# Optimization experiments

Measured on AMD Instinct MI355X. Metric: run time of the kernel, lower is better.

Reference implementation:

```python
import jax, jax.numpy as jnp
import numpy as np
from itertools import permutations

BLOCK = 64  # GroupLinear block_size


def _dist_bucket_table():
    # replicates self.distance: log2-style bucketing of token distances [0,1024)
    t = np.zeros(1024, dtype=np.int32)
    for i, th in enumerate([2, 4, 8, 16, 32, 64, 128, 256, 512]):
        t[th:] = i + 1
    return jnp.asarray(t)


def setup_inputs() -> dict:
    key = jax.random.key(0)
    ks = jax.random.split(key, 12)
    B, S, H, NH = 4, 512, 768, 12
    E, TAG, TE, TD, R = 24, 7, 20, 20, 97
    DIN = 2 * H + TE + TD
    hidden_state = jax.random.normal(ks[0], (B, S, H), jnp.float32)
    attention = jax.random.uniform(ks[1], (B, NH, S, S), jnp.float32)
    attention_mask = jnp.ones((B, S), jnp.float32)
    head = jnp.sort(jax.random.randint(ks[2], (B, E), 0, S), axis=-1)
    tail = jnp.sort(jax.random.randint(ks[3], (B, E), 0, S), axis=-1)
    entity_type = jax.random.randint(ks[4], (B, E), 0, TAG)
    type_table = jax.random.normal(ks[5], (TAG, TE), jnp.float32) * 0.02
    dis_table = jax.random.normal(ks[6], (20, TD), jnp.float32) * 0.02
    Wh = jax.random.normal(ks[7], (DIN, H), jnp.float32) * (1.0 / np.sqrt(DIN))
    bh = jnp.zeros((H,), jnp.float32)
    Wt = jax.random.normal(ks[8], (DIN, H), jnp.float32) * (1.0 / np.sqrt(DIN))
    bt = jnp.zeros((H,), jnp.float32)
    # GroupLinear weight reshaped to [n_blocks, BLOCK, BLOCK, R]
    clsW = jax.random.normal(ks[9], (H // BLOCK, BLOCK, BLOCK, R), jnp.float32) * (1.0 / np.sqrt(H * BLOCK))
    clsb = jnp.zeros((R,), jnp.float32)
    return dict(hidden_state=hidden_state, attention=attention,
                attention_mask=attention_mask, head=head, tail=tail,
                entity_type=entity_type, type_table=type_table,
                dis_table=dis_table, Wh=Wh, bh=bh, Wt=Wt, bt=bt,
                clsW=clsW, clsb=clsb)


def reference(hidden_state, attention, attention_mask, head, tail, entity_type,
              type_table, dis_table, Wh, bh, Wt, bt, clsW, clsb):
    E = head.shape[1]
    hts = jnp.asarray(list(permutations(range(E), 2)), dtype=jnp.int32)  # [P,2]
    i0, i1 = hts[:, 0], hts[:, 1]
    dtab = _dist_bucket_table()
    att = attention.sum(axis=1)  # [B,S,S] sum over heads

    def per_sample(h, a, m, hd, tl, et):
        # h:[S,H] a:[S,S] m:[S] hd,tl,et:[E]
        ent_feat = (h[hd] + h[tl]) * 0.5          # [E,H]
        ent_att = (a[hd] + a[tl]) * 0.5           # [E,S]
        ent_tf = type_table[et]                   # [E,TE]
        head_f, tail_f = ent_feat[i0], ent_feat[i1]      # [P,H]
        ht_att = ent_att[i0] * ent_att[i1] * m[None, :]  # [P,S]
        head_ty, tail_ty = ent_tf[i0], ent_tf[i1]        # [P,TE]
        d = dtab[jnp.abs(tl[i0] - hd[i1])]               # [P]
        ht_dist = dis_table[d]                           # [P,TD]
        ht_att = ht_att / (ht_att.sum(-1, keepdims=True) + 1e-20)
        ht_info = ht_att @ h                             # [P,H]
        all_h = jnp.concatenate([head_f, ht_info, head_ty, ht_dist], axis=-1)
        all_t = jnp.concatenate([tail_f, ht_info, tail_ty, ht_dist], axis=-1)
        return all_h, all_t

    all_h, all_t = jax.vmap(per_sample)(hidden_state, att, attention_mask,
                                        head, tail, entity_type)
    all_h = all_h.reshape(-1, all_h.shape[-1])  # [B*P, DIN]
    all_t = all_t.reshape(-1, all_t.shape[-1])
    h1 = jnp.tanh(all_h @ Wh + bh)              # [L,H]
    t1 = jnp.tanh(all_t @ Wt + bt)
    L, H = h1.shape
    nb = H // BLOCK
    x1 = h1.reshape(L, nb, BLOCK)
    x2 = t1.reshape(L, nb, BLOCK)
    # GroupLinear: per-block outer product then linear, fused as einsum
    logits = jnp.einsum('lnb,lnc,nbcr->lr', x1, x2, clsW) + clsb  # [L,R]
    return logits
```

## Files before the change

### kernel.cpp

```cpp
#include <hip/hip_runtime.h>
#include <hip/hip_bf16.h>
#include <math.h>

#define B_ 4
#define S_ 512
#define H_ 768
#define NH_ 12
#define E_ 24
#define TE_ 20
#define TD_ 20
#define R_ 97
#define DIN_ 1576
#define KPAD_ 1600
#define KS_MLP 50
#define KS_HTI 16
#define P_ 552
#define L_ 2208
#define NB_ 12
#define NF_ 7

typedef __bf16 bf16x8 __attribute__((ext_vector_type(8)));
typedef float f32x4 __attribute__((ext_vector_type(4)));

__device__ __forceinline__ unsigned short f2bf(float f) {
  union { float f; unsigned u; } c; c.f = f;
  unsigned r = c.u + 0x7FFF + ((c.u >> 16) & 1);
  return (unsigned short)(r >> 16);
}
__device__ __forceinline__ float bf2f(unsigned short b) {
  union { unsigned u; float f; } c; c.u = ((unsigned)b) << 16;
  return c.f;
}
__device__ __forceinline__ unsigned pk2(float a, float b) {
  return (unsigned)f2bf(a) | ((unsigned)f2bf(b) << 16);
}
__device__ __forceinline__ void gload_lds16(const uint4* g, uint4* l) {
  __builtin_amdgcn_global_load_lds(
      (const __attribute__((address_space(1))) unsigned*)(const void*)g,
      (__attribute__((address_space(3))) unsigned*)(void*)l, 16, 0, 0);
}

__global__ void ent_prep(const float* __restrict__ attn, const float* __restrict__ hs,
                         const int* __restrict__ head, const int* __restrict__ tail,
                         float* __restrict__ ent_att, float* __restrict__ ent_feat) {
  int be = blockIdx.x;
  int b = be / E_;
  int hd = head[be], tl = tail[be];
  int tid = threadIdx.x;
  const float* abase = attn + (size_t)b * NH_ * S_ * S_;
  for (int s = tid; s < S_; s += 256) {
    float acc = 0.f;
#pragma unroll
    for (int nh = 0; nh < NH_; ++nh) {
      const float* ap = abase + (size_t)nh * S_ * S_;
      acc += ap[(size_t)hd * S_ + s] + ap[(size_t)tl * S_ + s];
    }
    ent_att[(size_t)be * S_ + s] = 0.5f * acc;
  }
  const float* hb = hs + (size_t)b * S_ * H_;
  for (int k = tid; k < H_; k += 256) {
    ent_feat[(size_t)be * H_ + k] = 0.5f * (hb[(size_t)hd * H_ + k] + hb[(size_t)tl * H_ + k]);
  }
}

__global__ void pair_att(const float* __restrict__ ent_att, const float* __restrict__ mask,
                         const int* __restrict__ head, const int* __restrict__ tail,
                         const int* __restrict__ etype,
                         float* __restrict__ ht_att, int* __restrict__ meta) {
  int l = blockIdx.x;
  int b = l / P_, p = l % P_;
  int i0 = p / (E_ - 1), rem = p % (E_ - 1);
  int i1 = rem + (rem >= i0 ? 1 : 0);
  int tid = threadIdx.x;
  if (tid == 0) {
    meta[0 * L_ + l] = b * E_ + i0;
    meta[1 * L_ + l] = b * E_ + i1;
    meta[2 * L_ + l] = etype[b * E_ + i0];
    meta[3 * L_ + l] = etype[b * E_ + i1];
    int d = abs(tail[b * E_ + i0] - head[b * E_ + i1]);
    int bk = (d >= 2) + (d >= 4) + (d >= 8) + (d >= 16) + (d >= 32) +
             (d >= 64) + (d >= 128) + (d >= 256) + (d >= 512);
    meta[4 * L_ + l] = bk;
  }
  const float* a0 = ent_att + (size_t)(b * E_ + i0) * S_;
  const float* a1 = ent_att + (size_t)(b * E_ + i1) * S_;
  const float* m = mask + (size_t)b * S_;
  float v0 = a0[tid] * a1[tid] * m[tid];
  float v1 = a0[tid + 256] * a1[tid + 256] * m[tid + 256];
  float loc = v0 + v1;
  for (int o = 32; o > 0; o >>= 1) loc += __shfl_down(loc, o, 64);
  __shared__ float red[4];
  if ((tid & 63) == 0) red[tid >> 6] = loc;
  __syncthreads();
  float tot = red[0] + red[1] + red[2] + red[3];
  float inv = 1.f / (tot + 1e-20f);
  ht_att[(size_t)l * S_ + tid] = v0 * inv;
  ht_att[(size_t)l * S_ + tid + 256] = v1 * inv;
}

__global__ void pack_hs(const float* __restrict__ hs, uint4* __restrict__ hsP) {
  int u = blockIdx.x * 256 + threadIdx.x;
  if (u >= B_ * KS_HTI * 48 * 64) return;
  int lane = u & 63;
  int t = u >> 6;
  int nt16 = t % 48;
  int t2 = t / 48;
  int ks = t2 % KS_HTI;
  int b = t2 / KS_HTI;
  int n = nt16 * 16 + (lane & 15);
  int k0 = ks * 32 + ((lane >> 4) << 3);
  const float* src = hs + (size_t)b * S_ * H_;
  unsigned w[4];
#pragma unroll
  for (int q = 0; q < 4; ++q) {
    int k = k0 + 2 * q;
    w[q] = pk2(src[(size_t)k * H_ + n], src[(size_t)(k + 1) * H_ + n]);
  }
  uint4 o; o.x = w[0]; o.y = w[1]; o.z = w[2]; o.w = w[3];
  hsP[u] = o;
}

__global__ void pack_Wmlp(const float* __restrict__ Wh, const float* __restrict__ Wt,
                          uint4* __restrict__ WpH, uint4* __restrict__ WpT) {
  int u = blockIdx.x * 256 + threadIdx.x;
  if (u >= KS_MLP * 48 * 64) return;
  const float* W = blockIdx.y ? Wt : Wh;
  uint4* Wp = blockIdx.y ? WpT : WpH;
  int lane = u & 63;
  int t = u >> 6;
  int nt16 = t % 48;
  int ks = t / 48;
  int n = nt16 * 16 + (lane & 15);
  int k0 = ks * 32 + ((lane >> 4) << 3);
  unsigned w[4];
#pragma unroll
  for (int q = 0; q < 4; ++q) {
    int k = k0 + 2 * q;
    float v0 = (k < DIN_) ? W[(size_t)k * H_ + n] : 0.f;
    float v1 = (k + 1 < DIN_) ? W[(size_t)(k + 1) * H_ + n] : 0.f;
    w[q] = pk2(v0, v1);
  }
  uint4 o; o.x = w[0]; o.y = w[1]; o.z = w[2]; o.w = w[3];
  Wp[u] = o;
}

__global__ __launch_bounds__(256) void htinfo_mfma(
    const float* __restrict__ htatt, const uint4* __restrict__ hsP,
    float* __restrict__ htinfo) {
  int b = blockIdx.z;
  int m0 = blockIdx.x * 64;
  int n0 = blockIdx.y * 128;
  int tid = threadIdx.x;
  int wave = tid >> 6, lane = tid & 63;
  int wm = wave & 1, wn = wave >> 1;
  __shared__ __align__(16) unsigned short Ash[2][2048];
  __shared__ __align__(16) unsigned short Bsh[2][4096];

  int amt = tid >> 6, alane = tid & 63;
  int arow = m0 + amt * 16 + (alane & 15);
  bool rowok = arow < P_;
  const float* ap = htatt + ((size_t)b * P_ + (rowok ? arow : 0)) * S_;
  int akoff = (alane >> 4) << 3;
  int nt0 = n0 >> 4;

  f32x4 acc[2][4];
#pragma unroll
  for (int i = 0; i < 2; ++i)
#pragma unroll
    for (int j = 0; j < 4; ++j) acc[i][j] = (f32x4){0.f, 0.f, 0.f, 0.f};

  {
    uint4 aU; size_t gb = ((size_t)(b * KS_HTI + 0) * 48 + nt0) * 64;
    uint4 b0 = hsP[gb + tid], b1 = hsP[gb + 256 + tid];
    if (rowok) {
      float4 v0 = *(const float4*)(ap + akoff);
      float4 v1 = *(const float4*)(ap + akoff + 4);
      aU.x = pk2(v0.x, v0.y); aU.y = pk2(v0.z, v0.w);
      aU.z = pk2(v1.x, v1.y); aU.w = pk2(v1.z, v1.w);
    } else aU.x = aU.y = aU.z = aU.w = 0;
    *(uint4*)&Ash[0][tid * 8] = aU;
    *(uint4*)&Bsh[0][tid * 8] = b0;
    *(uint4*)&Bsh[0][tid * 8 + 2048] = b1;
  }
  __syncthreads();

  for (int ks = 0; ks < KS_HTI; ++ks) {
    int cur = ks & 1, nxt = cur ^ 1;
    bool more = (ks + 1 < KS_HTI);
    uint4 aN, bN0, bN1;
    if (more) {
      size_t gb = ((size_t)(b * KS_HTI + ks + 1) * 48 + nt0) * 64;
      bN0 = hsP[gb + tid]; bN1 = hsP[gb + 256 + tid];
      int k = (ks + 1) * 32 + akoff;
      if (rowok) {
        float4 v0 = *(const float4*)(ap + k);
        float4 v1 = *(const float4*)(ap + k + 4);
        aN.x = pk2(v0.x, v0.y); aN.y = pk2(v0.z, v0.w);
        aN.z = pk2(v1.x, v1.y); aN.w = pk2(v1.z, v1.w);
      } else aN.x = aN.y = aN.z = aN.w = 0;
    }
    bf16x8 af[2], bf[4];
#pragma unroll
    for (int mf = 0; mf < 2; ++mf)
      af[mf] = *(const bf16x8*)&Ash[cur][((wm * 2 + mf) * 64 + lane) * 8];
#pragma unroll
    for (int nf = 0; nf < 4; ++nf)
      bf[nf] = *(const bf16x8*)&Bsh[cur][((wn * 4 + nf) * 64 + lane) * 8];
#pragma unroll
    for (int nf = 0; nf < 4; ++nf)
#pragma unroll
      for (int mf = 0; mf < 2; ++mf)
        acc[mf][nf] = __builtin_amdgcn_mfma_f32_16x16x32_bf16(af[mf], bf[nf], acc[mf][nf], 0, 0, 0);
    if (more) {
      *(uint4*)&Ash[nxt][tid * 8] = aN;
      *(uint4*)&Bsh[nxt][tid * 8] = bN0;
      *(uint4*)&Bsh[nxt][tid * 8 + 2048] = bN1;
    }
    __syncthreads();
  }

#pragma unroll
  for (int mf = 0; mf < 2; ++mf)
#pragma unroll
    for (int nf = 0; nf < 4; ++nf) {
      int n = n0 + (wn * 4 + nf) * 16 + (lane & 15);
#pragma unroll
      for (int reg = 0; reg < 4; ++reg) {
        int l = m0 + (wm * 2 + mf) * 16 + ((lane >> 4) << 2) + reg;
        if (l < P_)
          htinfo[((size_t)b * P_ + l) * H_ + n] = acc[mf][nf][reg];
      }
    }
}

__global__ __launch_bounds__(256) void mlp_mfma(
    const float* __restrict__ ent_feat, const float* __restrict__ ht_info,
    const float* __restrict__ ttab, const float* __restrict__ dtab,
    const int* __restrict__ meta,
    const uint4* __restrict__ Wp_h, const uint4* __restrict__ Wp_t,
    const float* __restrict__ bh, const float* __restrict__ bt,
    float* __restrict__ h1, float* __restrict__ t1) {
  int half = blockIdx.z;
  const uint4* Wp = half ? Wp_t : Wp_h;
  const float* bias = half ? bt : bh;
  float* out = half ? t1 : h1;
  const int* feat_row = meta + half * L_;
  const int* type_row = meta + (2 + half) * L_;
  const int* distb = meta + 4 * L_;

  int l0 = blockIdx.x * 64;
  int n0 = blockIdx.y * 128;
  int tid = threadIdx.x;
  int wave = tid >> 6, lane = tid & 63;
  int wm = wave & 1, wn = wave >> 1;
  __shared__ __align__(16) unsigned short Ash[2][2048];
  __shared__ __align__(16) unsigned short Bsh[2][4096];

  int amt = tid >> 6, alane = tid & 63;
  int arow = l0 + amt * 16 + (alane & 15);
  bool rowok = arow < L_;
  int frow = 0, trow = 0, db = 0;
  if (rowok) { frow = feat_row[arow]; trow = type_row[arow]; db = distb[arow]; }
  const float* efp = ent_feat + (size_t)frow * H_;
  const float* hip_ = ht_info + (size_t)arow * H_;
  int akoff = (alane >> 4) << 3;
  int nt0 = n0 >> 4;

  f32x4 acc[2][4];
#pragma unroll
  for (int i = 0; i < 2; ++i)
#pragma unroll
    for (int j = 0; j < 4; ++j) acc[i][j] = (f32x4){0.f, 0.f, 0.f, 0.f};

  auto gatherA = [&](int ks, uint4& d) {
    int k = ks * 32 + akoff;
    if (!rowok) { d.x = d.y = d.z = d.w = 0; return; }
    if (k < 768) {
      float4 v0 = *(const float4*)(efp + k);
      float4 v1 = *(const float4*)(efp + k + 4);
      d.x = pk2(v0.x, v0.y); d.y = pk2(v0.z, v0.w);
      d.z = pk2(v1.x, v1.y); d.w = pk2(v1.z, v1.w);
    } else if (k < 1536) {
      float4 v0 = *(const float4*)(hip_ + k - 768);
      float4 v1 = *(const float4*)(hip_ + k - 764);
      d.x = pk2(v0.x, v0.y); d.y = pk2(v0.z, v0.w);
      d.z = pk2(v1.x, v1.y); d.w = pk2(v1.z, v1.w);
    } else {
      float v[8];
#pragma unroll
      for (int j = 0; j < 8; ++j) {
        int e = k + j;
        v[j] = (e < 1556) ? ttab[trow * TE_ + (e - 1536)]
             : (e < 1576) ? dtab[db * TD_ + (e - 1556)] : 0.f;
      }
      d.x = pk2(v[0], v[1]); d.y = pk2(v[2], v[3]);
      d.z = pk2(v[4], v[5]); d.w = pk2(v[6], v[7]);
    }
  };

  {
    uint4 aU; gatherA(0, aU);
    size_t gb = ((size_t)0 * 48 + nt0) * 64;
    uint4 b0 = Wp[gb + tid], b1 = Wp[gb + 256 + tid];
    *(uint4*)&Ash[0][tid * 8] = aU;
    *(uint4*)&Bsh[0][tid * 8] = b0;
    *(uint4*)&Bsh[0][tid * 8 + 2048] = b1;
  }
  __syncthreads();

  for (int ks = 0; ks < KS_MLP; ++ks) {
    int cur = ks & 1, nxt = cur ^ 1;
    bool more = (ks + 1 < KS_MLP);
    uint4 aN, bN0, bN1;
    if (more) {
      size_t gb = ((size_t)(ks + 1) * 48 + nt0) * 64;
      bN0 = Wp[gb + tid]; bN1 = Wp[gb + 256 + tid];
      gatherA(ks + 1, aN);
    }
    bf16x8 af[2], bf[4];
#pragma unroll
    for (int mf = 0; mf < 2; ++mf)
      af[mf] = *(const bf16x8*)&Ash[cur][((wm * 2 + mf) * 64 + lane) * 8];
#pragma unroll
    for (int nf = 0; nf < 4; ++nf)
      bf[nf] = *(const bf16x8*)&Bsh[cur][((wn * 4 + nf) * 64 + lane) * 8];
#pragma unroll
    for (int nf = 0; nf < 4; ++nf)
#pragma unroll
      for (int mf = 0; mf < 2; ++mf)
        acc[mf][nf] = __builtin_amdgcn_mfma_f32_16x16x32_bf16(af[mf], bf[nf], acc[mf][nf], 0, 0, 0);
    if (more) {
      *(uint4*)&Ash[nxt][tid * 8] = aN;
      *(uint4*)&Bsh[nxt][tid * 8] = bN0;
      *(uint4*)&Bsh[nxt][tid * 8 + 2048] = bN1;
    }
    __syncthreads();
  }

#pragma unroll
  for (int mf = 0; mf < 2; ++mf)
#pragma unroll
    for (int nf = 0; nf < 4; ++nf) {
      int n = n0 + (wn * 4 + nf) * 16 + (lane & 15);
      float bv = bias[n];
#pragma unroll
      for (int reg = 0; reg < 4; ++reg) {
        int l = l0 + (wm * 2 + mf) * 16 + ((lane >> 4) << 2) + reg;
        if (l < L_)
          out[(size_t)l * H_ + n] = tanhf(acc[mf][nf][reg] + bv);
      }
    }
}

__global__ void pack_w(const float* __restrict__ clsW, uint4* __restrict__ Wfrag) {
  int nb = blockIdx.x;
  __shared__ float Wls[64][98];
  int tid = threadIdx.x;
  const float* src = clsW + (size_t)nb * 64 * R_;
  for (int idx = tid; idx < 64 * R_; idx += 256) {
    Wls[idx / R_][idx % R_] = src[idx];
  }
  __syncthreads();
  for (int u = tid; u < 896; u += 256) {
    int nf = u >> 7;
    int kc = (u >> 6) & 1;
    int lane = u & 63;
    int r = (lane & 15) + 16 * nf;
    unsigned w[4];
#pragma unroll
    for (int q = 0; q < 4; ++q) {
      int c0 = ((lane >> 4) << 3) + 2 * q + 32 * kc;
      float v0 = (r < R_) ? Wls[c0][r] : 0.f;
      float v1 = (r < R_) ? Wls[c0 + 1][r] : 0.f;
      w[q] = (unsigned)f2bf(v0) | ((unsigned)f2bf(v1) << 16);
    }
    uint4 o; o.x = w[0]; o.y = w[1]; o.z = w[2]; o.w = w[3];
    Wfrag[(size_t)nb * 896 + u] = o;
  }
}

__global__ __launch_bounds__(256) void bilinear_mfma(
    const float* __restrict__ h1, const float* __restrict__ t1,
    const uint4* __restrict__ Wfrag, float* __restrict__ part) {
  int n = blockIdx.y;
  int l0 = blockIdx.x * 64;
  int tid = threadIdx.x;
  int wave = tid >> 6, lane = tid & 63;
  int wm = wave & 1, kh = wave >> 1;
  __shared__ __align__(16) uint4 Wl[2][2][896];
  __shared__ unsigned short x1s[64][64];

  for (int i = tid; i < 1024; i += 256) {
    int l = i >> 4, bq = (i & 15) * 4;
    float4 v = make_float4(0, 0, 0, 0);
    if (l0 + l < L_) v = *(const float4*)(h1 + (size_t)(l0 + l) * H_ + n * 64 + bq);
    x1s[bq + 0][l] = f2bf(v.x);
    x1s[bq + 1][l] = f2bf(v.y);
    x1s[bq + 2][l] = f2bf(v.z);
    x1s[bq + 3][l] = f2bf(v.w);
  }

  float x2f[2][2][8];
#pragma unroll
  for (int mf = 0; mf < 2; ++mf) {
    int row = l0 + wm * 32 + mf * 16 + (lane & 15);
#pragma unroll
    for (int kc = 0; kc < 2; ++kc) {
      float4 v0 = make_float4(0, 0, 0, 0), v1 = v0;
      if (row < L_) {
        const float* p = t1 + (size_t)row * H_ + n * 64 + kc * 32 + ((lane >> 4) << 3);
        v0 = *(const float4*)p;
        v1 = *(const float4*)(p + 4);
      }
      x2f[mf][kc][0] = v0.x; x2f[mf][kc][1] = v0.y;
      x2f[mf][kc][2] = v0.z; x2f[mf][kc][3] = v0.w;
      x2f[mf][kc][4] = v1.x; x2f[mf][kc][5] = v1.y;
      x2f[mf][kc][6] = v1.z; x2f[mf][kc][7] = v1.w;
    }
  }

  f32x4 acc[2][NF_];
#pragma unroll
  for (int mf = 0; mf < 2; ++mf)
#pragma unroll
    for (int nf = 0; nf < NF_; ++nf)
      acc[mf][nf] = (f32x4){0.f, 0.f, 0.f, 0.f};

  const uint4* gbase = Wfrag + (size_t)n * 64 * 896;
  auto stage = [&](int b, int buf) {
    const uint4* gs = gbase + (size_t)b * 896 + (wm * 7) * 64 + lane;
#pragma unroll
    for (int r = 0; r < 7; ++r)
      gload_lds16(gs + r * 64, &Wl[kh][buf][(wm * 7 + r) * 64]);
  };

  stage(kh * 32, 0);
  __syncthreads();

  for (int s = 0; s < 32; ++s) {
    int b = kh * 32 + s;
    int cur = s & 1, nxt = cur ^ 1;
    if (s + 1 < 32) stage(b + 1, nxt);
    bf16x8 afr[2][2];
#pragma unroll
    for (int mf = 0; mf < 2; ++mf) {
      float x1v = bf2f(x1s[b][wm * 32 + mf * 16 + (lane & 15)]);
#pragma unroll
      for (int kc = 0; kc < 2; ++kc)
#pragma unroll
        for (int j = 0; j < 8; ++j)
          afr[mf][kc][j] = (__bf16)(x1v * x2f[mf][kc][j]);
    }
#pragma unroll
    for (int nf = 0; nf < NF_; ++nf) {
#pragma unroll
      for (int kc = 0; kc < 2; ++kc) {
        bf16x8 bfr = *(const bf16x8*)&Wl[kh][cur][(nf * 2 + kc) * 64 + lane];
#pragma unroll
        for (int mf = 0; mf < 2; ++mf)
          acc[mf][nf] = __builtin_amdgcn_mfma_f32_16x16x32_bf16(
              afr[mf][kc], bfr, acc[mf][nf], 0, 0, 0);
      }
    }
    __syncthreads();
  }

  float* red = (float*)&Wl[0][0][0];
  int rbase = (wm * 64 + lane) * 68;
  if (kh == 1) {
#pragma unroll
    for (int mf = 0; mf < 2; ++mf)
#pragma unroll
      for (int nf = 0; nf < NF_; ++nf)
        *(f32x4*)&red[rbase + (mf * NF_ + nf) * 4] = acc[mf][nf];
  }
  __syncthreads();
  if (kh == 0) {
#pragma unroll
    for (int mf = 0; mf < 2; ++mf)
#pragma unroll
      for (int nf = 0; nf < NF_; ++nf)
        acc[mf][nf] += *(const f32x4*)&red[rbase + (mf * NF_ + nf) * 4];
#pragma unroll
    for (int mf = 0; mf < 2; ++mf) {
#pragma unroll
      for (int nf = 0; nf < NF_; ++nf) {
        int r = nf * 16 + (lane & 15);
        if (r < R_) {
#pragma unroll
          for (int reg = 0; reg < 4; ++reg) {
            int l = l0 + wm * 32 + mf * 16 + ((lane >> 4) << 2) + reg;
            if (l < L_)
              part[((size_t)n * L_ + l) * R_ + r] = acc[mf][nf][reg];
          }
        }
      }
    }
  }
}

__global__ void reduce_logits(const float* __restrict__ part, const float* __restrict__ clsb,
                              float* __restrict__ out) {
  int idx = blockIdx.x * 256 + threadIdx.x;
  if (idx < L_ * R_) {
    int r = idx % R_;
    float s = clsb[r];
#pragma unroll
    for (int nn = 0; nn < NB_; ++nn) s += part[(size_t)nn * L_ * R_ + idx];
    out[idx] = s;
  }
}

extern "C" void kernel_launch(void* const* d_in, const int* in_sizes, int n_in,
                              void* d_out, int out_size, void* d_ws, size_t ws_size,
                              hipStream_t stream) {
  const float* hs   = (const float*)d_in[0];
  const float* attn = (const float*)d_in[1];
  const float* mask = (const float*)d_in[2];
  const int*   head = (const int*)d_in[3];
  const int*   tail = (const int*)d_in[4];
  const int*   etyp = (const int*)d_in[5];
  const float* ttab = (const float*)d_in[6];
  const float* dtab = (const float*)d_in[7];
  const float* Wh   = (const float*)d_in[8];
  const float* bh   = (const float*)d_in[9];
  const float* Wt   = (const float*)d_in[10];
  const float* bt   = (const float*)d_in[11];
  const float* clsW = (const float*)d_in[12];
  const float* clsb = (const float*)d_in[13];
  float* out = (float*)d_out;

  float* ws = (float*)d_ws;
  float* ent_att  = ws; ws += (size_t)B_ * E_ * S_;
  float* ent_feat = ws; ws += (size_t)B_ * E_ * H_;
  float* ht_att   = ws; ws += (size_t)L_ * S_;
  float* ht_info  = ws; ws += (size_t)L_ * H_;
  float* h1       = ws; ws += (size_t)L_ * H_;
  float* t1       = ws; ws += (size_t)L_ * H_;
  float* part     = ws; ws += (size_t)NB_ * L_ * R_;
  int* meta = (int*)ws;

  uint4* Wpack_h = (uint4*)ht_att;
  uint4* Wpack_t = (uint4*)part;
  uint4* hsPack  = (uint4*)(part + (size_t)1048576);
  uint4* Wfrag   = (uint4*)ht_att;

  ent_prep<<<B_ * E_, 256, 0, stream>>>(attn, hs, head, tail, ent_att, ent_feat);
  pair_att<<<L_, 256, 0, stream>>>(ent_att, mask, head, tail, etyp, ht_att, meta);
  pack_hs<<<(B_ * KS_HTI * 48 * 64) / 256, 256, 0, stream>>>(hs, hsPack);
  htinfo_mfma<<<dim3(9, 6, B_), 256, 0, stream>>>(ht_att, hsPack, ht_info);
  pack_Wmlp<<<dim3((KS_MLP * 48 * 64) / 256, 2), 256, 0, stream>>>(Wh, Wt, Wpack_h, Wpack_t);
  mlp_mfma<<<dim3(35, 6, 2), 256, 0, stream>>>(ent_feat, ht_info, ttab, dtab, meta,
      Wpack_h, Wpack_t, bh, bt, h1, t1);
  pack_w<<<NB_ * 64, 256, 0, stream>>>(clsW, Wfrag);
  bilinear_mfma<<<dim3(35, NB_), 256, 0, stream>>>(h1, t1, Wfrag, part);
  reduce_logits<<<(L_ * R_ + 255) / 256, 256, 0, stream>>>(part, clsb, out);
}
```

Measured before the change: 143.5 us.

## Halve GEMM N-tile and stage B tiles with direct global-to-LDS loads

```diff
diff --git a/kernel.cpp b/kernel.cpp
--- a/kernel.cpp
+++ b/kernel.cpp
@@ -149,12 +149,12 @@
     float* __restrict__ htinfo) {
   int b = blockIdx.z;
   int m0 = blockIdx.x * 64;
-  int n0 = blockIdx.y * 128;
+  int n0 = blockIdx.y * 64;
   int tid = threadIdx.x;
   int wave = tid >> 6, lane = tid & 63;
   int wm = wave & 1, wn = wave >> 1;
   __shared__ __align__(16) unsigned short Ash[2][2048];
-  __shared__ __align__(16) unsigned short Bsh[2][4096];
+  __shared__ __align__(16) uint4 Bsh[2][256];
 
   int amt = tid >> 6, alane = tid & 63;
   int arow = m0 + amt * 16 + (alane & 15);
@@ -163,67 +163,62 @@
   int akoff = (alane >> 4) << 3;
   int nt0 = n0 >> 4;
 
-  f32x4 acc[2][4];
+  f32x4 acc[2][2];
 #pragma unroll
   for (int i = 0; i < 2; ++i)
 #pragma unroll
-    for (int j = 0; j < 4; ++j) acc[i][j] = (f32x4){0.f, 0.f, 0.f, 0.f};
+    for (int j = 0; j < 2; ++j) acc[i][j] = (f32x4){0.f, 0.f, 0.f, 0.f};
+
+  auto stageB = [&](int ks, int buf) {
+    const uint4* gs = hsP + ((size_t)(b * KS_HTI + ks) * 48 + nt0 + wave) * 64 + lane;
+    gload_lds16(gs, &Bsh[buf][wave * 64]);
+  };
+  auto gatherA = [&](int ks, uint4& d) {
+    if (!rowok) { d.x = d.y = d.z = d.w = 0; return; }
+    int k = ks * 32 + akoff;
+    float4 v0 = *(const float4*)(ap + k);
+    float4 v1 = *(const float4*)(ap + k + 4);
+    d.x = pk2(v0.x, v0.y); d.y = pk2(v0.z, v0.w);
+    d.z = pk2(v1.x, v1.y); d.w = pk2(v1.z, v1.w);
+  };
 
   {
-    uint4 aU; size_t gb = ((size_t)(b * KS_HTI + 0) * 48 + nt0) * 64;
-    uint4 b0 = hsP[gb + tid], b1 = hsP[gb + 256 + tid];
-    if (rowok) {
-      float4 v0 = *(const float4*)(ap + akoff);
-      float4 v1 = *(const float4*)(ap + akoff + 4);
-      aU.x = pk2(v0.x, v0.y); aU.y = pk2(v0.z, v0.w);
-      aU.z = pk2(v1.x, v1.y); aU.w = pk2(v1.z, v1.w);
-    } else aU.x = aU.y = aU.z = aU.w = 0;
+    stageB(0, 0);
+    uint4 aU; gatherA(0, aU);
     *(uint4*)&Ash[0][tid * 8] = aU;
-    *(uint4*)&Bsh[0][tid * 8] = b0;
-    *(uint4*)&Bsh[0][tid * 8 + 2048] = b1;
   }
   __syncthreads();
 
   for (int ks = 0; ks < KS_HTI; ++ks) {
     int cur = ks & 1, nxt = cur ^ 1;
     bool more = (ks + 1 < KS_HTI);
-    uint4 aN, bN0, bN1;
+    uint4 aN;
     if (more) {
-      size_t gb = ((size_t)(b * KS_HTI + ks + 1) * 48 + nt0) * 64;
-      bN0 = hsP[gb + tid]; bN1 = hsP[gb + 256 + tid];
-      int k = (ks + 1) * 32 + akoff;
-      if (rowok) {
-        float4 v0 = *(const float4*)(ap + k);
-        float4 v1 = *(const float4*)(ap + k + 4);
-        aN.x = pk2(v0.x, v0.y); aN.y = pk2(v0.z, v0.w);
-        aN.z = pk2(v1.x, v1.y); aN.w = pk2(v1.z, v1.w);
-      } else aN.x = aN.y = aN.z = aN.w = 0;
-    }
-    bf16x8 af[2], bf[4];
+      stageB(ks + 1, nxt);
+      gatherA(ks + 1, aN);
+    }
+    bf16x8 af[2], bf[2];
 #pragma unroll
     for (int mf = 0; mf < 2; ++mf)
       af[mf] = *(const bf16x8*)&Ash[cur][((wm * 2 + mf) * 64 + lane) * 8];
 #pragma unroll
-    for (int nf = 0; nf < 4; ++nf)
-      bf[nf] = *(const bf16x8*)&Bsh[cur][((wn * 4 + nf) * 64 + lane) * 8];
-#pragma unroll
-    for (int nf = 0; nf < 4; ++nf)
+    for (int nf = 0; nf < 2; ++nf)
+      bf[nf] = *(const bf16x8*)&Bsh[cur][(wn * 2 + nf) * 64 + lane];
+#pragma unroll
+    for (int nf = 0; nf < 2; ++nf)
 #pragma unroll
       for (int mf = 0; mf < 2; ++mf)
         acc[mf][nf] = __builtin_amdgcn_mfma_f32_16x16x32_bf16(af[mf], bf[nf], acc[mf][nf], 0, 0, 0);
-    if (more) {
+    if (more)
       *(uint4*)&Ash[nxt][tid * 8] = aN;
-      *(uint4*)&Bsh[nxt][tid * 8] = bN0;
-      *(uint4*)&Bsh[nxt][tid * 8 + 2048] = bN1;
-    }
     __syncthreads();
   }
 
 #pragma unroll
   for (int mf = 0; mf < 2; ++mf)
 #pragma unroll
-    for (int nf = 0; nf < 4; ++nf) {
-      int n = n0 + (wn * 4 + nf) * 16 + (lane & 15);
+    for (int nf = 0; nf < 2; ++nf) {
+      int n = n0 + (wn * 2 + nf) * 16 + (lane & 15);
 #pragma unroll
       for (int reg = 0; reg < 4; ++reg) {
         int l = m0 + (wm * 2 + mf) * 16 + ((lane >> 4) << 2) + reg;
@@ -249,12 +244,12 @@
   const int* distb = meta + 4 * L_;
 
   int l0 = blockIdx.x * 64;
-  int n0 = blockIdx.y * 128;
+  int n0 = blockIdx.y * 64;
   int tid = threadIdx.x;
   int wave = tid >> 6, lane = tid & 63;
   int wm = wave & 1, wn = wave >> 1;
   __shared__ __align__(16) unsigned short Ash[2][2048];
-  __shared__ __align__(16) unsigned short Bsh[2][4096];
+  __shared__ __align__(16) uint4 Bsh[2][256];
 
   int amt = tid >> 6, alane = tid & 63;
   int arow = l0 + amt * 16 + (alane & 15);
@@ -266,12 +261,16 @@
   int akoff = (alane >> 4) << 3;
   int nt0 = n0 >> 4;
 
-  f32x4 acc[2][4];
+  f32x4 acc[2][2];
 #pragma unroll
   for (int i = 0; i < 2; ++i)
 #pragma unroll
-    for (int j = 0; j < 4; ++j) acc[i][j] = (f32x4){0.f, 0.f, 0.f, 0.f};
-
+    for (int j = 0; j < 2; ++j) acc[i][j] = (f32x4){0.f, 0.f, 0.f, 0.f};
+
+  auto stageB = [&](int ks, int buf) {
+    const uint4* gs = Wp + ((size_t)ks * 48 + nt0 + wave) * 64 + lane;
+    gload_lds16(gs, &Bsh[buf][wave * 64]);
+  };
   auto gatherA = [&](int ks, uint4& d) {
     int k = ks * 32 + akoff;
     if (!rowok) { d.x = d.y = d.z = d.w = 0; return; }
@@ -299,49 +298,42 @@
   };
 
   {
+    stageB(0, 0);
     uint4 aU; gatherA(0, aU);
-    size_t gb = ((size_t)0 * 48 + nt0) * 64;
-    uint4 b0 = Wp[gb + tid], b1 = Wp[gb + 256 + tid];
     *(uint4*)&Ash[0][tid * 8] = aU;
-    *(uint4*)&Bsh[0][tid * 8] = b0;
-    *(uint4*)&Bsh[0][tid * 8 + 2048] = b1;
   }
   __syncthreads();
 
   for (int ks = 0; ks < KS_MLP; ++ks) {
     int cur = ks & 1, nxt = cur ^ 1;
     bool more = (ks + 1 < KS_MLP);
-    uint4 aN, bN0, bN1;
+    uint4 aN;
     if (more) {
-      size_t gb = ((size_t)(ks + 1) * 48 + nt0) * 64;
-      bN0 = Wp[gb + tid]; bN1 = Wp[gb + 256 + tid];
+      stageB(ks + 1, nxt);
       gatherA(ks + 1, aN);
     }
-    bf16x8 af[2], bf[4];
+    bf16x8 af[2], bf[2];
 #pragma unroll
     for (int mf = 0; mf < 2; ++mf)
       af[mf] = *(const bf16x8*)&Ash[cur][((wm * 2 + mf) * 64 + lane) * 8];
 #pragma unroll
-    for (int nf = 0; nf < 4; ++nf)
-      bf[nf] = *(const bf16x8*)&Bsh[cur][((wn * 4 + nf) * 64 + lane) * 8];
-#pragma unroll
-    for (int nf = 0; nf < 4; ++nf)
+    for (int nf = 0; nf < 2; ++nf)
+      bf[nf] = *(const bf16x8*)&Bsh[cur][(wn * 2 + nf) * 64 + lane];
+#pragma unroll
+    for (int nf = 0; nf < 2; ++nf)
 #pragma unroll
       for (int mf = 0; mf < 2; ++mf)
         acc[mf][nf] = __builtin_amdgcn_mfma_f32_16x16x32_bf16(af[mf], bf[nf], acc[mf][nf], 0, 0, 0);
-    if (more) {
+    if (more)
       *(uint4*)&Ash[nxt][tid * 8] = aN;
-      *(uint4*)&Bsh[nxt][tid * 8] = bN0;
-      *(uint4*)&Bsh[nxt][tid * 8 + 2048] = bN1;
-    }
     __syncthreads();
   }
 
 #pragma unroll
   for (int mf = 0; mf < 2; ++mf)
 #pragma unroll
-    for (int nf = 0; nf < 4; ++nf) {
-      int n = n0 + (wn * 4 + nf) * 16 + (lane & 15);
+    for (int nf = 0; nf < 2; ++nf) {
+      int n = n0 + (wn * 2 + nf) * 16 + (lane & 15);
       float bv = bias[n];
 #pragma unroll
       for (int reg = 0; reg < 4; ++reg) {
@@ -548,9 +540,9 @@
   ent_prep<<<B_ * E_, 256, 0, stream>>>(attn, hs, head, tail, ent_att, ent_feat);
   pair_att<<<L_, 256, 0, stream>>>(ent_att, mask, head, tail, etyp, ht_att, meta);
   pack_hs<<<(B_ * KS_HTI * 48 * 64) / 256, 256, 0, stream>>>(hs, hsPack);
-  htinfo_mfma<<<dim3(9, 6, B_), 256, 0, stream>>>(ht_att, hsPack, ht_info);
+  htinfo_mfma<<<dim3(9, 12, B_), 256, 0, stream>>>(ht_att, hsPack, ht_info);
   pack_Wmlp<<<dim3((KS_MLP * 48 * 64) / 256, 2), 256, 0, stream>>>(Wh, Wt, Wpack_h, Wpack_t);
-  mlp_mfma<<<dim3(35, 6, 2), 256, 0, stream>>>(ent_feat, ht_info, ttab, dtab, meta,
+  mlp_mfma<<<dim3(35, 12, 2), 256, 0, stream>>>(ent_feat, ht_info, ttab, dtab, meta,
       Wpack_h, Wpack_t, bh, bt, h1, t1);
   pack_w<<<NB_ * 64, 256, 0, stream>>>(clsW, Wfrag);
   bilinear_mfma<<<dim3(35, NB_), 256, 0, stream>>>(h1, t1, Wfrag, part);
```

Result: no change. 141.9 us (-1.1%).
